# Kernel tuning notes

Measured on AMD Instinct MI355X. Metric: run time of the kernel, lower is better.

## Reference

```python
import jax, jax.numpy as jnp
import numpy as np

LATENT = 256
HEADS = 4
DIM_HEAD = 256            # dim_head = latent_channels
INNER = HEADS * DIM_HEAD  # 1024
ROT_DIM = DIM_HEAD // 2   # rotary dim per coordinate (relative_emb_dim=2)
MIN_FREQ = 1.0 / 64.0     # 1/res
ROT_SCALE = 16.0          # CrossFormer scale
FF_SCALE = 0.5            # Gaussian Fourier feature scale
PI = 3.141592653589793
OUT_CH = 3


def _gelu(x):
    return jax.nn.gelu(x, approximate=False)  # torch nn.GELU default (erf)


def _rot_freqs(coords, dim):
    # coords: [b, n] -> freqs [b, n, dim]
    inv_freq = 1.0 / (10000.0 ** (jnp.arange(0, dim, 2, dtype=jnp.float32) / dim))
    t = coords * (ROT_SCALE / MIN_FREQ)
    f = t[..., None] * inv_freq               # [b, n, dim//2]
    return jnp.concatenate([f, f], axis=-1)    # [b, n, dim]


def _rotate_half(x):
    x1, x2 = jnp.split(x, 2, axis=-1)
    return jnp.concatenate([-x2, x1], axis=-1)


def _apply_rot(t, freqs):
    return t * jnp.cos(freqs) + _rotate_half(t) * jnp.sin(freqs)


def _apply_2d_rot(t, fx, fy):
    d = t.shape[-1]
    tx, ty = t[..., : d // 2], t[..., d // 2 :]
    return jnp.concatenate([_apply_rot(tx, fx), _apply_rot(ty, fy)], axis=-1)


def _inst_norm(t, eps=1e-5):
    # galerkin normalization: non-affine norm over head dim (InstanceNorm1d, affine=False)
    mu = jnp.mean(t, axis=-1, keepdims=True)
    var = jnp.var(t, axis=-1, keepdims=True)
    return (t - mu) * jax.lax.rsqrt(var + eps)


def setup_inputs() -> dict:
    key = jax.random.key(0)
    ks = jax.random.split(key, 20)
    b, nq, nc = 8, 4096, 4096
    s = 0.02
    return {
        "z": jax.random.normal(ks[0], (b, nc, LATENT), jnp.float32),
        "query_pos": jax.random.uniform(ks[1], (b, nq, 2), jnp.float32),
        "context_pos": jax.random.uniform(ks[2], (b, nc, 2), jnp.float32),
        # GaussianFourierFeatureTransform buffer B: [2, mapping_size=latent/2]
        "B_ff": jax.random.normal(ks[3], (2, LATENT // 2), jnp.float32) * FF_SCALE,
        # coordinate_projection linears (bias=False)
        "Wc1": jax.random.normal(ks[4], (LATENT, LATENT), jnp.float32) * s,
        "Wc2": jax.random.normal(ks[5], (LATENT, LATENT), jnp.float32) * s,
        # cross attention projections
        "Wq": jax.random.normal(ks[6], (LATENT, INNER), jnp.float32) * s,
        "Wkv": jax.random.normal(ks[7], (LATENT, 2 * INNER), jnp.float32) * s,
        "Wo": jax.random.normal(ks[8], (INNER, LATENT), jnp.float32) * s,
        "bo": jnp.zeros((LATENT,), jnp.float32),
        # feed-forward (mlp_dim = latent)
        "Wf1": jax.random.normal(ks[9], (LATENT, LATENT), jnp.float32) * s,
        "bf1": jnp.zeros((LATENT,), jnp.float32),
        "Wf2": jax.random.normal(ks[10], (LATENT, LATENT), jnp.float32) * s,
        "bf2": jnp.zeros((LATENT,), jnp.float32),
        # output head
        "Wh1": jax.random.normal(ks[11], (LATENT + 2, LATENT), jnp.float32) * s,
        "Wh2": jax.random.normal(ks[12], (LATENT, LATENT // 2), jnp.float32) * s,
        "Wh3": jax.random.normal(ks[13], (LATENT // 2, OUT_CH), jnp.float32) * s,
        "bh3": jnp.zeros((OUT_CH,), jnp.float32),
    }


def reference(z, query_pos, context_pos, B_ff, Wc1, Wc2, Wq, Wkv, Wo, bo,
              Wf1, bf1, Wf2, bf2, Wh1, Wh2, Wh3, bh3):
    b, nq, _ = query_pos.shape
    nc = z.shape[1]
    # 1) Gaussian Fourier features + 2-layer projection
    ff = 2.0 * PI * (query_pos @ B_ff)                           # [b, nq, latent/2]
    x = jnp.concatenate([jnp.sin(ff), jnp.cos(ff)], axis=-1)      # [b, nq, latent]
    x = _gelu(x @ Wc1) @ Wc2
    # 2) galerkin cross attention with 2D rotary relative pos emb
    q = (x @ Wq).reshape(b, nq, HEADS, DIM_HEAD).transpose(0, 2, 1, 3)
    k, v = jnp.split(z @ Wkv, 2, axis=-1)
    k = k.reshape(b, nc, HEADS, DIM_HEAD).transpose(0, 2, 1, 3)
    v = v.reshape(b, nc, HEADS, DIM_HEAD).transpose(0, 2, 1, 3)
    fxq = _rot_freqs(query_pos[..., 0], ROT_DIM)[:, None]         # [b,1,nq,rot]
    fyq = _rot_freqs(query_pos[..., 1], ROT_DIM)[:, None]
    fxk = _rot_freqs(context_pos[..., 0], ROT_DIM)[:, None]
    fyk = _rot_freqs(context_pos[..., 1], ROT_DIM)[:, None]
    q = _apply_2d_rot(q, fxq, fyq)
    k = _apply_2d_rot(k, fxk, fyk)
    k = _inst_norm(k)
    v = _inst_norm(v)
    kv = jnp.einsum('bhnd,bhne->bhde', k, v)                      # [b,h,d,d]
    attn = jnp.einsum('bhmd,bhde->bhme', q, kv) * (1.0 / nc)      # [b,h,nq,d]
    attn = attn.transpose(0, 2, 1, 3).reshape(b, nq, INNER)
    x = (attn @ Wo + bo) + x                                      # residual
    x = (_gelu(x @ Wf1 + bf1) @ Wf2 + bf2) + x                    # FFN residual
    # 3) output head on [features, coords]
    h = jnp.concatenate([x, query_pos], axis=-1)
    h = _gelu(h @ Wh1)
    h = _gelu(h @ Wh2)
    return h @ Wh3 + bh3                                          # [b, nq, out_ch]
```

## Files before the change

### kernel.cpp

```cpp
#include <hip/hip_runtime.h>
#include <math.h>


typedef unsigned short u16;
typedef __attribute__((ext_vector_type(4))) float f32x4;
typedef __attribute__((ext_vector_type(8))) short s16x8;
typedef __attribute__((ext_vector_type(8))) unsigned short u16x8;
typedef __attribute__((ext_vector_type(4))) unsigned short u16x4;

#define LOG2_1E4_D64 0.20762050593046013f

__device__ __forceinline__ u16 f2b(float f){
  union { float f; unsigned u; } v; v.f = f;
  unsigned u = v.u;
  u += 0x7FFFu + ((u >> 16) & 1u);
  return (u16)(u >> 16);
}
__device__ __forceinline__ float b2f(u16 b){
  union { unsigned u; float f; } v; v.u = ((unsigned)b) << 16; return v.f;
}
__device__ __forceinline__ float gelu_f(float x){
  return 0.5f * x * (1.0f + erff(x * 0.7071067811865475f));
}

#if __has_builtin(__builtin_amdgcn_global_load_lds)
#define HAVE_GLL 1
typedef const __attribute__((address_space(1))) void* as1cv;
typedef __attribute__((address_space(3))) void* as3v;
__device__ __forceinline__ void gload16(const void* g, void* l){
  __builtin_amdgcn_global_load_lds((as1cv)g, (as3v)l, 16, 0, 0);
}
#else
#define HAVE_GLL 0
#endif


__global__ __launch_bounds__(256) void k_cast(const float* __restrict__ in, u16* __restrict__ out){
  long i = (long)blockIdx.x * 256 + threadIdx.x;
  float4 f = ((const float4*)in)[i];
  u16x4 o = { f2b(f.x), f2b(f.y), f2b(f.z), f2b(f.w) };
  ((u16x4*)out)[i] = o;
}

struct TCArgs {
  const float* W[9]; u16* Wt[9];
  int K[9]; int N[9]; int boff[10];
};
__global__ __launch_bounds__(256) void k_tcast_all(TCArgs a){
  int b = blockIdx.x;
  int w = 0;
  while (b >= a.boff[w+1]) w++;
  int idx = (b - a.boff[w]) * 256 + threadIdx.x;
  int K = a.K[w], N = a.N[w];
  int n = idx / K, k = idx - n * K;
  a.Wt[w][idx] = f2b(a.W[w][(long)k * N + n]);
}

__global__ __launch_bounds__(256) void k_fourier(const float* __restrict__ qp, const float* __restrict__ Bff, u16* __restrict__ X0){
  int tid = threadIdx.x;
  long r = (long)blockIdx.x * 2 + (tid >> 7);
  int j = tid & 127;
  float qx = qp[r*2], qy = qp[r*2+1];
  float ff = 6.283185307179586f * (qx * Bff[j] + qy * Bff[128 + j]);
  X0[r*256 + j]       = f2b(sinf(ff));
  X0[r*256 + 128 + j] = f2b(cosf(ff));
}

__global__ __launch_bounds__(256) void k_red(const float* __restrict__ p, u16* __restrict__ out, long stride){
  long i = (long)blockIdx.x * 256 + threadIdx.x;
  f32x4 s = ((const f32x4*)p)[i];
  s += ((const f32x4*)(p + stride))[i];
  s += ((const f32x4*)(p + 2*stride))[i];
  s += ((const f32x4*)(p + 3*stride))[i];
  u16x4 o = { f2b(s[0]), f2b(s[1]), f2b(s[2]), f2b(s[3]) };
  ((u16x4*)out)[i] = o;
}

__global__ __launch_bounds__(256) void k_final(const u16* __restrict__ H2, const float* __restrict__ Wh3,
                                               const float* __restrict__ bh3, float* __restrict__ out){
  long r = (long)blockIdx.x * 256 + threadIdx.x;
  float a0 = bh3[0], a1 = bh3[1], a2 = bh3[2];
  const u16x8* hrow = (const u16x8*)(H2 + r*128);
#pragma unroll
  for (int c8 = 0; c8 < 16; c8++){
    u16x8 hv = hrow[c8];
#pragma unroll
    for (int e = 0; e < 8; e++){
      float f = b2f(hv[e]);
      int k = c8*8 + e;
      a0 += f * Wh3[k*3];
      a1 += f * Wh3[k*3+1];
      a2 += f * Wh3[k*3+2];
    }
  }
  out[r*3] = a0; out[r*3+1] = a1; out[r*3+2] = a2;
}


template<int MODE>
__global__ __launch_bounds__(256, 2)
void gemm_fuse(const u16* __restrict__ A, const u16* __restrict__ Bw,
               u16* __restrict__ outK, u16* __restrict__ outV,
               const float* __restrict__ pos){
  __shared__ char smem[49152];
  u16* AsB[2] = { (u16*)smem,            (u16*)(smem + 8192)  };
  u16* BsB[2] = { (u16*)(smem + 16384),  (u16*)(smem + 32768) };

  int tid  = threadIdx.x;
  int lane = tid & 63;
  int wave = tid >> 6;
  int wm = (wave & 1) << 6;
  int wn = (wave >> 1) << 7;
  int whalf = wave >> 1;
  int yb = blockIdx.x;
  int h  = yb & 3;
  bool isK = (MODE == 1) || (yb < 4);
  long m0 = (long)blockIdx.y * 128;

  int r15 = lane & 15;
  int cc  = lane >> 4;
  const u16* Bh = Bw + (long)yb * 65536;

  int srow = lane >> 2;
  int scol = (lane & 3) * 8;
  int aRow[2], bRow[4];
  const u16 *gA[2], *gB[4];
#pragma unroll
  for (int t = 0; t < 2; t++){
    aRow[t] = (wave*2 + t) * 16;
    gA[t] = A + (m0 + aRow[t] + srow) * 256 + scol;
  }
#pragma unroll
  for (int t = 0; t < 4; t++){
    bRow[t] = (wave*4 + t) * 16;
    gB[t] = Bh + (bRow[t] + srow) * 256 + scol;
  }

  f32x4 acc[4][8];
#pragma unroll
  for (int i = 0; i < 4; i++)
#pragma unroll
    for (int j = 0; j < 8; j++)
      acc[i][j] = f32x4{0.f, 0.f, 0.f, 0.f};

#if HAVE_GLL
#pragma unroll
  for (int t = 0; t < 2; t++) gload16(gA[t], AsB[0] + aRow[t]*32);
#pragma unroll
  for (int t = 0; t < 4; t++) gload16(gB[t], BsB[0] + bRow[t]*32);
  __syncthreads();
  int cur = 0;
  for (int k0 = 0; k0 < 256; k0 += 32){
    int nxt = cur ^ 1;
    if (k0 < 224){
#pragma unroll
      for (int t = 0; t < 2; t++) gload16(gA[t] + k0 + 32, AsB[nxt] + aRow[t]*32);
#pragma unroll
      for (int t = 0; t < 4; t++) gload16(gB[t] + k0 + 32, BsB[nxt] + bRow[t]*32);
    }
    s16x8 af[4], bf[8];
#pragma unroll
    for (int i = 0; i < 4; i++) af[i] = *(const s16x8*)&AsB[cur][(wm + i*16 + r15)*32 + cc*8];
#pragma unroll
    for (int j = 0; j < 8; j++) bf[j] = *(const s16x8*)&BsB[cur][(wn + j*16 + r15)*32 + cc*8];
#pragma unroll
    for (int i = 0; i < 4; i++)
#pragma unroll
      for (int j = 0; j < 8; j++)
        acc[i][j] = __builtin_amdgcn_mfma_f32_16x16x32_bf16(af[i], bf[j], acc[i][j], 0, 0, 0);
    __syncthreads();
    cur = nxt;
  }
#else
  int sm = tid >> 2, sc = tid & 3;
  for (int k0 = 0; k0 < 256; k0 += 32){
    u16x8 va  = *(const u16x8*)(A + (m0 + sm)*256 + sc*8 + k0);
    u16x8 va1 = *(const u16x8*)(A + (m0 + sm + 64)*256 + sc*8 + k0);
    u16x8 vb0 = *(const u16x8*)(Bh + (sm      )*256 + sc*8 + k0);
    u16x8 vb1 = *(const u16x8*)(Bh + (sm + 64 )*256 + sc*8 + k0);
    u16x8 vb2 = *(const u16x8*)(Bh + (sm + 128)*256 + sc*8 + k0);
    u16x8 vb3 = *(const u16x8*)(Bh + (sm + 192)*256 + sc*8 + k0);
    __syncthreads();
    *(u16x8*)&AsB[0][sm*32 + sc*8] = va;
    *(u16x8*)&AsB[0][(sm+64)*32 + sc*8] = va1;
    *(u16x8*)&BsB[0][sm*32 + sc*8] = vb0;
    *(u16x8*)&BsB[0][(sm+64)*32 + sc*8] = vb1;
    *(u16x8*)&BsB[1][sm*32 + sc*8] = vb2;
    *(u16x8*)&BsB[1][(sm+64)*32 + sc*8] = vb3;
    __syncthreads();
    s16x8 af[4], bf[8];
#pragma unroll
    for (int i = 0; i < 4; i++) af[i] = *(const s16x8*)&AsB[0][(wm + i*16 + r15)*32 + cc*8];
#pragma unroll
    for (int j = 0; j < 8; j++){
      int rr = wn + j*16 + r15;
      bf[j] = (rr < 128) ? *(const s16x8*)&BsB[0][rr*32 + cc*8]
                         : *(const s16x8*)&BsB[1][(rr-128)*32 + cc*8];
    }
#pragma unroll
    for (int i = 0; i < 4; i++)
#pragma unroll
      for (int j = 0; j < 8; j++)
        acc[i][j] = __builtin_amdgcn_mfma_f32_16x16x32_bf16(af[i], bf[j], acc[i][j], 0, 0, 0);
    __syncthreads();
  }
#endif

  if (isK){
    float invf4[4];
#pragma unroll
    for (int jl = 0; jl < 4; jl++)
      invf4[jl] = 1024.0f * exp2f(-(float)(jl*16 + r15) * LOG2_1E4_D64);
#pragma unroll
    for (int i = 0; i < 4; i++){
#pragma unroll
      for (int r = 0; r < 4; r++){
        long n = m0 + wm + i*16 + cc*4 + r;
        float p = pos[n*2 + whalf];
#pragma unroll
        for (int jl = 0; jl < 4; jl++){
          float a = p * invf4[jl];
          float s = __sinf(a), c = __cosf(a);
          float t0 = acc[i][jl][r], t1 = acc[i][jl+4][r];
          acc[i][jl][r]   = t0*c - t1*s;
          acc[i][jl+4][r] = t1*c + t0*s;
        }
      }
    }
  }

  if constexpr (MODE == 1){
#pragma unroll
    for (int i = 0; i < 4; i++)
#pragma unroll
      for (int j = 0; j < 8; j++)
#pragma unroll
        for (int r = 0; r < 4; r++){
          long row = m0 + wm + i*16 + cc*4 + r;
          int col = yb*256 + wn + j*16 + r15;
          outK[row*1024 + col] = f2b(acc[i][j][r]);
        }
  } else {
    u16*   TB  = (u16*)smem;
    float* PS1 = (float*)(smem + 32768);
    float* PS2 = (float*)(smem + 33792);

#pragma unroll
    for (int i = 0; i < 4; i++){
#pragma unroll
      for (int r = 0; r < 4; r++){
        float s1 = 0.f, s2 = 0.f;
#pragma unroll
        for (int j = 0; j < 8; j++){
          float v = acc[i][j][r];
          s1 += v; s2 += v*v;
        }
#pragma unroll
        for (int m = 1; m < 16; m <<= 1){
          s1 += __shfl_xor(s1, m, 64);
          s2 += __shfl_xor(s2, m, 64);
        }
        int rowid = (wave&1)*64 + i*16 + cc*4 + r;
        if (r15 == 0){ PS1[whalf*128 + rowid] = s1; PS2[whalf*128 + rowid] = s2; }
      }
    }
    __syncthreads();
#pragma unroll
    for (int i = 0; i < 4; i++){
#pragma unroll
      for (int r = 0; r < 4; r++){
        int rowid = (wave&1)*64 + i*16 + cc*4 + r;
        float s1 = PS1[rowid] + PS1[128 + rowid];
        float s2 = PS2[rowid] + PS2[128 + rowid];
        float mu  = s1 * 0.00390625f;
        float var = s2 * 0.00390625f - mu*mu;
        float inv = 1.0f / sqrtf(var + 1e-5f);
#pragma unroll
        for (int j = 0; j < 8; j++)
          acc[i][j][r] = (acc[i][j][r] - mu) * inv;
      }
    }
    __syncthreads();

    u16* outp = isK ? outK : outV;
    int bb  = (int)(m0 >> 12);
    int nn0 = (int)(m0 & 4095);
    long matbase = ((long)(bb*4 + h) * 256) * 4096;
#pragma unroll
    for (int p = 0; p < 2; p++){
      if ((wave & 1) == p){
#pragma unroll
        for (int i = 0; i < 4; i++)
#pragma unroll
          for (int j = 0; j < 8; j++)
#pragma unroll
            for (int r = 0; r < 4; r++){
              int nl = i*16 + cc*4 + r;
              int d  = wn + j*16 + r15;
              TB[nl*256 + (d ^ ((nl>>2)<<1))] = f2b(acc[i][j][r]);
            }
      }
      __syncthreads();
      {
        int n4 = (lane & 15) * 4;
        int sw = (lane & 15) << 1;
#pragma unroll
        for (int rnd = 0; rnd < 16; rnd++){
          int d = rnd*16 + wave*4 + (lane >> 4);
          u16x4 vv;
#pragma unroll
          for (int jj = 0; jj < 4; jj++) vv[jj] = TB[(n4+jj)*256 + (d ^ sw)];
          *(u16x4*)(outp + matbase + (long)d*4096 + nn0 + p*64 + n4) = vv;
        }
      }
      __syncthreads();
    }
  }
}


enum { EP_B = 0, EP_GELU = 1, EP_BIAS_GELU = 2, EP_BIAS_RESB = 3, EP_SCALE = 4,
       EP_QP_GELU = 5, EP_F32 = 6 };

struct GArgs {
  const u16* A; const u16* B;
  u16* Cb; float* Cf;
  const float* bias; const u16* res; const float* qp; const float* wtail;
  float scale;
  int M, N, K, lda, ldb, ldc, NLO;
  long sAh, sAl, sBh, sBl, sCh, sCl;
};

template<int EP>
__global__ __launch_bounds__(256, 2)
void gemm_k(GArgs g){
  int z = blockIdx.z;
  int zh = z / g.NLO, zl = z - zh * g.NLO;
  const u16* A = g.A + (long)zh * g.sAh + (long)zl * g.sAl;
  const u16* B = g.B + (long)zh * g.sBh + (long)zl * g.sBl;
  long coff = (long)zh * g.sCh + (long)zl * g.sCl;

  __shared__ u16 As[2][128*32];
  __shared__ u16 Bs[2][128*32];

  int tid  = threadIdx.x;
  int lane = tid & 63;
  int wave = tid >> 6;
  int wm = (wave & 1) << 6;
  int wn = (wave >> 1) << 6;
  long m0 = (long)blockIdx.x * 128;
  long n0 = (long)blockIdx.y * 128;

  int r15 = lane & 15;
  int cc  = lane >> 4;

  f32x4 acc[4][4];
#pragma unroll
  for (int i = 0; i < 4; i++)
#pragma unroll
    for (int j = 0; j < 4; j++)
      acc[i][j] = f32x4{0.f, 0.f, 0.f, 0.f};

#if HAVE_GLL
  int srow = lane >> 2;
  int scol = (lane & 3) * 8;
  int aRow[2];
  const u16 *gA[2], *gB[2];
#pragma unroll
  for (int t = 0; t < 2; t++){
    aRow[t] = (wave*2 + t) * 16;
    gA[t] = A + (m0 + aRow[t] + srow) * g.lda + scol;
    gB[t] = B + (n0 + aRow[t] + srow) * g.ldb + scol;
  }
#pragma unroll
  for (int t = 0; t < 2; t++){ gload16(gA[t], As[0] + aRow[t]*32); gload16(gB[t], Bs[0] + aRow[t]*32); }
  __syncthreads();
  int cur = 0;
  for (int k0 = 0; k0 < g.K; k0 += 32){
    int nxt = cur ^ 1;
    if (k0 + 32 < g.K){
#pragma unroll
      for (int t = 0; t < 2; t++){
        gload16(gA[t] + k0 + 32, As[nxt] + aRow[t]*32);
        gload16(gB[t] + k0 + 32, Bs[nxt] + aRow[t]*32);
      }
    }
    s16x8 af[4], bf[4];
#pragma unroll
    for (int i = 0; i < 4; i++) af[i] = *(const s16x8*)&As[cur][(wm + i*16 + r15)*32 + cc*8];
#pragma unroll
    for (int i = 0; i < 4; i++) bf[i] = *(const s16x8*)&Bs[cur][(wn + i*16 + r15)*32 + cc*8];
#pragma unroll
    for (int i = 0; i < 4; i++)
#pragma unroll
      for (int j = 0; j < 4; j++)
        acc[i][j] = __builtin_amdgcn_mfma_f32_16x16x32_bf16(af[i], bf[j], acc[i][j], 0, 0, 0);
    __syncthreads();
    cur = nxt;
  }
#else
  int sm  = tid >> 2;
  int sc  = tid & 3;
  for (int k0 = 0; k0 < g.K; k0 += 32){
    u16x8 va0 = *(const u16x8*)(A + (m0 + sm )*g.lda + sc*8 + k0);
    u16x8 va1 = *(const u16x8*)(A + (m0 + sm + 64)*g.lda + sc*8 + k0);
    u16x8 vb0 = *(const u16x8*)(B + (n0 + sm )*g.ldb + sc*8 + k0);
    u16x8 vb1 = *(const u16x8*)(B + (n0 + sm + 64)*g.ldb + sc*8 + k0);
    __syncthreads();
    *(u16x8*)&As[0][sm*32 + sc*8] = va0;
    *(u16x8*)&As[0][(sm+64)*32 + sc*8] = va1;
    *(u16x8*)&Bs[0][sm*32 + sc*8] = vb0;
    *(u16x8*)&Bs[0][(sm+64)*32 + sc*8] = vb1;
    __syncthreads();
    s16x8 af[4], bf[4];
#pragma unroll
    for (int i = 0; i < 4; i++) af[i] = *(const s16x8*)&As[0][(wm + i*16 + r15)*32 + cc*8];
#pragma unroll
    for (int i = 0; i < 4; i++) bf[i] = *(const s16x8*)&Bs[0][(wn + i*16 + r15)*32 + cc*8];
#pragma unroll
    for (int i = 0; i < 4; i++)
#pragma unroll
      for (int j = 0; j < 4; j++)
        acc[i][j] = __builtin_amdgcn_mfma_f32_16x16x32_bf16(af[i], bf[j], acc[i][j], 0, 0, 0);
    __syncthreads();
  }
#endif

  int colb = (int)n0 + wn + r15;
  int rowb = (int)m0 + wm + cc * 4;
#pragma unroll
  for (int i = 0; i < 4; i++){
#pragma unroll
    for (int j = 0; j < 4; j++){
      int col = colb + j*16;
#pragma unroll
      for (int r = 0; r < 4; r++){
        int row = rowb + i*16 + r;
        float v = acc[i][j][r];
        if constexpr (EP == EP_B){
          g.Cb[coff + (long)row * g.ldc + col] = f2b(v);
        } else if constexpr (EP == EP_GELU){
          g.Cb[coff + (long)row * g.ldc + col] = f2b(gelu_f(v));
        } else if constexpr (EP == EP_BIAS_GELU){
          v = gelu_f(v + g.bias[col]);
          g.Cb[coff + (long)row * g.ldc + col] = f2b(v);
        } else if constexpr (EP == EP_BIAS_RESB){
          v += g.bias[col] + b2f(g.res[(long)row * g.ldc + col]);
          g.Cb[coff + (long)row * g.ldc + col] = f2b(v);
        } else if constexpr (EP == EP_SCALE){
          g.Cb[coff + (long)row * g.ldc + col] = f2b(v * g.scale);
        } else if constexpr (EP == EP_F32){
          g.Cf[coff + (long)row * g.ldc + col] = v;
        } else {
          v += g.qp[(long)row*2] * g.wtail[col] + g.qp[(long)row*2+1] * g.wtail[256+col];
          g.Cb[coff + (long)row * g.ldc + col] = f2b(gelu_f(v));
        }
      }
    }
  }
}


extern "C" void kernel_launch(void* const* d_in, const int* in_sizes, int n_in,
                              void* d_out, int out_size, void* d_ws, size_t ws_size,
                              hipStream_t stream){
  const float* z   = (const float*)d_in[0];
  const float* qp  = (const float*)d_in[1];
  const float* cp  = (const float*)d_in[2];
  const float* Bff = (const float*)d_in[3];
  const float* Wc1 = (const float*)d_in[4];
  const float* Wc2 = (const float*)d_in[5];
  const float* Wq  = (const float*)d_in[6];
  const float* Wkv = (const float*)d_in[7];
  const float* Wo  = (const float*)d_in[8];
  const float* bo  = (const float*)d_in[9];
  const float* Wf1 = (const float*)d_in[10];
  const float* bf1 = (const float*)d_in[11];
  const float* Wf2 = (const float*)d_in[12];
  const float* bf2 = (const float*)d_in[13];
  const float* Wh1 = (const float*)d_in[14];
  const float* Wh2 = (const float*)d_in[15];
  const float* Wh3 = (const float*)d_in[16];
  const float* bh3 = (const float*)d_in[17];
  float* out = (float*)d_out;
  (void)in_sizes; (void)n_in; (void)out_size;

  size_t mb = ws_size >> 20;
  int C;
  if      (mb >= 264) C = 1;
  else if (mb >= 168) C = 2;
  else if (mb >= 120) C = 4;
  else                C = 8;
  const int NB = 8 / C;
  const long R = (long)NB * 4096;

  char* ws = (char*)d_ws;
  const size_t MB = 1024*1024;
  u16* WqT  = (u16*)(ws + 0);
  u16* WkvT = (u16*)(ws + 512*1024);
  u16* WoT  = (u16*)(ws + 1536*1024);
  u16* Wc1T = (u16*)(ws + 2048*1024);
  u16* Wc2T = (u16*)(ws + (2048+128)*1024);
  u16* Wf1T = (u16*)(ws + (2048+256)*1024);
  u16* Wf2T = (u16*)(ws + (2048+384)*1024);
  u16* Wh1T = (u16*)(ws + (2048+512)*1024);
  u16* Wh2T = (u16*)(ws + (2048+640)*1024);
  u16* R1 = (u16*)(ws + 4*MB);
  u16* R2 = (u16*)(ws + 20*MB);
  u16* R3 = (u16*)(ws + 36*MB);
  u16* R4 = (u16*)(ws + 52*MB);
  u16* kvT = (u16*)(ws + 68*MB);
  u16* BIG1 = (u16*)(ws + 72*MB);
  u16* BIG2 = (u16*)((char*)BIG1 + (size_t)NB*8*MB);
  u16* BIG3 = (u16*)((char*)BIG2 + (size_t)NB*8*MB);

  u16* X0b = R1; u16* X2b = R1;
  u16* Tb  = R2; u16* H1b = R2;
  u16* Xb  = R3;
  u16* Zb  = R4; u16* H2b = R4;

  auto G = [&](int ep, const u16* A, const u16* B, u16* Cb, float* Cf,
               const float* bias, const u16* res, const float* qq, const float* wtail,
               float scale, int M, int N, int K, int lda, int ldb, int ldc,
               int nz, int NLO, long sAh, long sAl, long sBh, long sBl, long sCh, long sCl){
    GArgs g;
    g.A=A; g.B=B; g.Cb=Cb; g.Cf=Cf; g.bias=bias; g.res=res; g.qp=qq; g.wtail=wtail;
    g.scale=scale; g.M=M; g.N=N; g.K=K; g.lda=lda; g.ldb=ldb; g.ldc=ldc; g.NLO=NLO;
    g.sAh=sAh; g.sAl=sAl; g.sBh=sBh; g.sBl=sBl; g.sCh=sCh; g.sCl=sCl;
    dim3 gr(M/128, N/128, nz); dim3 bl(256);
    switch(ep){
      case EP_B:          gemm_k<EP_B><<<gr,bl,0,stream>>>(g); break;
      case EP_GELU:       gemm_k<EP_GELU><<<gr,bl,0,stream>>>(g); break;
      case EP_BIAS_GELU:  gemm_k<EP_BIAS_GELU><<<gr,bl,0,stream>>>(g); break;
      case EP_BIAS_RESB:  gemm_k<EP_BIAS_RESB><<<gr,bl,0,stream>>>(g); break;
      case EP_SCALE:      gemm_k<EP_SCALE><<<gr,bl,0,stream>>>(g); break;
      case EP_QP_GELU:    gemm_k<EP_QP_GELU><<<gr,bl,0,stream>>>(g); break;
      case EP_F32:        gemm_k<EP_F32><<<gr,bl,0,stream>>>(g); break;
    }
  };

  k_cast<<<dim3(8192), dim3(256), 0, stream>>>(z, Zb);
  {
    TCArgs a;
    const float* Ws[9] = { Wq, Wkv, Wo, Wc1, Wc2, Wf1, Wf2, Wh1, Wh2 };
    u16* Wts[9] = { WqT, WkvT, WoT, Wc1T, Wc2T, Wf1T, Wf2T, Wh1T, Wh2T };
    int Ks[9] = { 256, 256, 1024, 256, 256, 256, 256, 256, 256 };
    int Ns[9] = { 1024, 2048, 256, 256, 256, 256, 256, 256, 128 };
    int off = 0;
    for (int i = 0; i < 9; i++){
      a.W[i] = Ws[i]; a.Wt[i] = Wts[i]; a.K[i] = Ks[i]; a.N[i] = Ns[i];
      a.boff[i] = off; off += Ks[i]*Ns[i]/256;
    }
    a.boff[9] = off;
    k_tcast_all<<<dim3(off), dim3(256), 0, stream>>>(a);
  }

  k_fourier<<<dim3(16384), dim3(256), 0, stream>>>(qp, Bff, X0b);
  G(EP_GELU, X0b, Wc1T, Tb, 0, 0,0,0,0, 1.f, 32768,256,256, 256,256,256, 1,1, 0,0,0,0,0,0);
  G(EP_B,    Tb,  Wc2T, Xb, 0, 0,0,0,0, 1.f, 32768,256,256, 256,256,256, 1,1, 0,0,0,0,0,0);

  for (int c = 0; c < C; c++){
    long row0 = (long)c * R;
    const u16* Zc = Zb + row0 * 256;
    gemm_fuse<0><<<dim3(8, (int)(R/128)), dim3(256), 0, stream>>>(Zc, WkvT, BIG2, BIG3, cp + row0*2);
    G(EP_F32, BIG3, BIG2, 0, (float*)BIG1, 0,0,0,0, 1.f,
      256,256,1024, 4096,4096,256, 4*NB*4, NB*4,
      1024,1048576, 1024,1048576, (long)NB*4*65536,65536);
    k_red<<<dim3(NB*256), dim3(256), 0, stream>>>((float*)BIG1, kvT + (long)c*NB*4*65536, (long)NB*4*65536);
    gemm_fuse<1><<<dim3(4, (int)(R/128)), dim3(256), 0, stream>>>(Xb + row0*256, WqT, BIG1, 0, qp + row0*2);
    G(EP_SCALE, BIG1, kvT + (long)c*NB*4*65536, BIG2, 0, 0,0,0,0, 1.0f/4096.0f,
      4096,256,256, 1024,256,1024, NB*4,4, 4194304,256, 262144,65536, 4194304,256);
    G(EP_BIAS_RESB, BIG2, WoT, X2b + row0*256, 0, bo, Xb + row0*256, 0,0, 1.f,
      (int)R,256,1024, 1024,1024,256, 1,1, 0,0,0,0,0,0);
  }

  G(EP_BIAS_GELU, X2b, Wf1T, Tb, 0, bf1, 0,0,0, 1.f, 32768,256,256, 256,256,256, 1,1, 0,0,0,0,0,0);
  G(EP_BIAS_RESB, Tb, Wf2T, Xb, 0, bf2, X2b, 0,0, 1.f, 32768,256,256, 256,256,256, 1,1, 0,0,0,0,0,0);
  G(EP_QP_GELU, Xb, Wh1T, H1b, 0, 0,0, qp, Wh1 + 65536, 1.f, 32768,256,256, 256,256,256, 1,1, 0,0,0,0,0,0);
  G(EP_GELU, H1b, Wh2T, H2b, 0, 0,0,0,0, 1.f, 32768,128,256, 256,256,128, 1,1, 0,0,0,0,0,0);
  k_final<<<dim3(128), dim3(256), 0, stream>>>(H2b, Wh3, bh3, out);
}
```

Before: 540.4 us.

## Deepen GEMM prefetch with vmcnt waits, swizzle LDS, merge prep kernels

The GEMM main loops now stage two k-tiles ahead and wait on explicit vmcnt counters with raw barriers, instead of a full __syncthreads after every tile. This lets global-to-LDS loads overlap compute for longer. LDS columns are XOR-swizzled on both the load and fragment-read side to cut bank conflicts. The z cast, weight transpose-cast and Fourier feature kernels are merged into one prep launch to save launch overhead. The hand-written waitcnt/sched_barrier sequencing is fragile, so an extra sync was added before the epilogue reuses shared memory.

Measured after the change: 526.6 us. -2.6%, faster.

```diff
diff --git a/kernel.cpp b/kernel.cpp
--- a/kernel.cpp
+++ b/kernel.cpp
@@ -9,6 +9,11 @@
 typedef __attribute__((ext_vector_type(4))) unsigned short u16x4;
 
 #define LOG2_1E4_D64 0.20762050593046013f
+
+#define VMCNT(n) do{ asm volatile("s_waitcnt vmcnt(" #n ")" ::: "memory"); \
+                     __builtin_amdgcn_sched_barrier(0); }while(0)
+#define BARRIER() do{ __builtin_amdgcn_s_barrier(); \
+                      __builtin_amdgcn_sched_barrier(0); }while(0)
 
 __device__ __forceinline__ u16 f2b(float f){
   union { float f; unsigned u; } v; v.f = f;
@@ -35,35 +40,37 @@
 #endif
 
 
-__global__ __launch_bounds__(256) void k_cast(const float* __restrict__ in, u16* __restrict__ out){
-  long i = (long)blockIdx.x * 256 + threadIdx.x;
-  float4 f = ((const float4*)in)[i];
-  u16x4 o = { f2b(f.x), f2b(f.y), f2b(f.z), f2b(f.w) };
-  ((u16x4*)out)[i] = o;
-}
-
-struct TCArgs {
+struct PrepArgs {
+  const float* z; u16* Zb;
+  const float* qp; const float* Bff; u16* X0;
   const float* W[9]; u16* Wt[9];
   int K[9]; int N[9]; int boff[10];
+  int castB, tcB;
 };
-__global__ __launch_bounds__(256) void k_tcast_all(TCArgs a){
-  int b = blockIdx.x;
-  int w = 0;
-  while (b >= a.boff[w+1]) w++;
-  int idx = (b - a.boff[w]) * 256 + threadIdx.x;
-  int K = a.K[w], N = a.N[w];
-  int n = idx / K, k = idx - n * K;
-  a.Wt[w][idx] = f2b(a.W[w][(long)k * N + n]);
-}
-
-__global__ __launch_bounds__(256) void k_fourier(const float* __restrict__ qp, const float* __restrict__ Bff, u16* __restrict__ X0){
-  int tid = threadIdx.x;
-  long r = (long)blockIdx.x * 2 + (tid >> 7);
-  int j = tid & 127;
-  float qx = qp[r*2], qy = qp[r*2+1];
-  float ff = 6.283185307179586f * (qx * Bff[j] + qy * Bff[128 + j]);
-  X0[r*256 + j]       = f2b(sinf(ff));
-  X0[r*256 + 128 + j] = f2b(cosf(ff));
+__global__ __launch_bounds__(256) void k_prep(PrepArgs a){
+  int b = blockIdx.x, tid = threadIdx.x;
+  if (b < a.castB){
+    long i = (long)b * 256 + tid;
+    float4 f = ((const float4*)a.z)[i];
+    u16x4 o = { f2b(f.x), f2b(f.y), f2b(f.z), f2b(f.w) };
+    ((u16x4*)a.Zb)[i] = o;
+  } else if (b < a.castB + a.tcB){
+    int bb = b - a.castB;
+    int w = 0;
+    while (bb >= a.boff[w+1]) w++;
+    int idx = (bb - a.boff[w]) * 256 + tid;
+    int K = a.K[w], N = a.N[w];
+    int n = idx / K, k = idx - n * K;
+    a.Wt[w][idx] = f2b(a.W[w][(long)k * N + n]);
+  } else {
+    int bb = b - a.castB - a.tcB;
+    long r = (long)bb * 2 + (tid >> 7);
+    int j = tid & 127;
+    float qx = a.qp[r*2], qy = a.qp[r*2+1];
+    float ff = 6.283185307179586f * (qx * a.Bff[j] + qy * a.Bff[128 + j]);
+    a.X0[r*256 + j]       = f2b(sinf(ff));
+    a.X0[r*256 + 128 + j] = f2b(cosf(ff));
+  }
 }
 
 __global__ __launch_bounds__(256) void k_red(const float* __restrict__ p, u16* __restrict__ out, long stride){
@@ -103,8 +110,8 @@
                u16* __restrict__ outK, u16* __restrict__ outV,
                const float* __restrict__ pos){
   __shared__ char smem[49152];
-  u16* AsB[2] = { (u16*)smem,            (u16*)(smem + 8192)  };
-  u16* BsB[2] = { (u16*)(smem + 16384),  (u16*)(smem + 32768) };
+  u16* AsB = (u16*)smem;
+  u16* BsB = (u16*)(smem + 16384);
 
   int tid  = threadIdx.x;
   int lane = tid & 63;
@@ -119,58 +126,69 @@
 
   int r15 = lane & 15;
   int cc  = lane >> 4;
+  int fsw = (cc ^ ((r15 >> 1) & 3)) * 8;
   const u16* Bh = Bw + (long)yb * 65536;
 
-  int srow = lane >> 2;
-  int scol = (lane & 3) * 8;
+  f32x4 acc[4][8];
+#pragma unroll
+  for (int i = 0; i < 4; i++)
+#pragma unroll
+    for (int j = 0; j < 8; j++)
+      acc[i][j] = f32x4{0.f, 0.f, 0.f, 0.f};
+
+#if HAVE_GLL
+  int srow  = lane >> 2;
+  int scolS = ((lane & 3) ^ ((lane >> 3) & 3)) * 8;
   int aRow[2], bRow[4];
   const u16 *gA[2], *gB[4];
 #pragma unroll
   for (int t = 0; t < 2; t++){
     aRow[t] = (wave*2 + t) * 16;
-    gA[t] = A + (m0 + aRow[t] + srow) * 256 + scol;
+    gA[t] = A + (m0 + aRow[t] + srow) * 256 + scolS;
   }
 #pragma unroll
   for (int t = 0; t < 4; t++){
     bRow[t] = (wave*4 + t) * 16;
-    gB[t] = Bh + (bRow[t] + srow) * 256 + scol;
-  }
-
-  f32x4 acc[4][8];
-#pragma unroll
-  for (int i = 0; i < 4; i++)
-#pragma unroll
-    for (int j = 0; j < 8; j++)
-      acc[i][j] = f32x4{0.f, 0.f, 0.f, 0.f};
-
-#if HAVE_GLL
-#pragma unroll
-  for (int t = 0; t < 2; t++) gload16(gA[t], AsB[0] + aRow[t]*32);
-#pragma unroll
-  for (int t = 0; t < 4; t++) gload16(gB[t], BsB[0] + bRow[t]*32);
-  __syncthreads();
-  int cur = 0;
-  for (int k0 = 0; k0 < 256; k0 += 32){
-    int nxt = cur ^ 1;
-    if (k0 < 224){
-#pragma unroll
-      for (int t = 0; t < 2; t++) gload16(gA[t] + k0 + 32, AsB[nxt] + aRow[t]*32);
-#pragma unroll
-      for (int t = 0; t < 4; t++) gload16(gB[t] + k0 + 32, BsB[nxt] + bRow[t]*32);
-    }
+    gB[t] = Bh + (bRow[t] + srow) * 256 + scolS;
+  }
+  auto stage = [&](int buf, int kk){
+    u16* ab = AsB + buf*4096;
+    u16* bb = BsB + buf*8192;
+#pragma unroll
+    for (int t = 0; t < 2; t++) gload16(gA[t] + kk*32, ab + aRow[t]*32);
+#pragma unroll
+    for (int t = 0; t < 4; t++) gload16(gB[t] + kk*32, bb + bRow[t]*32);
+  };
+  auto compute = [&](int buf){
+    const u16* ab = AsB + buf*4096;
+    const u16* bb = BsB + buf*8192;
     s16x8 af[4], bf[8];
 #pragma unroll
-    for (int i = 0; i < 4; i++) af[i] = *(const s16x8*)&AsB[cur][(wm + i*16 + r15)*32 + cc*8];
-#pragma unroll
-    for (int j = 0; j < 8; j++) bf[j] = *(const s16x8*)&BsB[cur][(wn + j*16 + r15)*32 + cc*8];
+    for (int i = 0; i < 4; i++) af[i] = *(const s16x8*)&ab[(wm + i*16 + r15)*32 + fsw];
+#pragma unroll
+    for (int j = 0; j < 8; j++) bf[j] = *(const s16x8*)&bb[(wn + j*16 + r15)*32 + fsw];
 #pragma unroll
     for (int i = 0; i < 4; i++)
 #pragma unroll
       for (int j = 0; j < 8; j++)
         acc[i][j] = __builtin_amdgcn_mfma_f32_16x16x32_bf16(af[i], bf[j], acc[i][j], 0, 0, 0);
-    __syncthreads();
-    cur = nxt;
-  }
+  };
+
+  stage(0, 0);
+  stage(1, 1);
+  int cur = 0;
+  for (int t = 0; t < 7; t++){
+    VMCNT(6);
+    BARRIER();
+    compute(cur);
+    __builtin_amdgcn_sched_barrier(0);
+    BARRIER();
+    if (t + 2 < 8) stage(cur, t + 2);
+    cur ^= 1;
+  }
+  VMCNT(0);
+  BARRIER();
+  compute(cur);
 #else
   int sm = tid >> 2, sc = tid & 3;
   for (int k0 = 0; k0 < 256; k0 += 32){
@@ -181,22 +199,18 @@
     u16x8 vb2 = *(const u16x8*)(Bh + (sm + 128)*256 + sc*8 + k0);
     u16x8 vb3 = *(const u16x8*)(Bh + (sm + 192)*256 + sc*8 + k0);
     __syncthreads();
-    *(u16x8*)&AsB[0][sm*32 + sc*8] = va;
-    *(u16x8*)&AsB[0][(sm+64)*32 + sc*8] = va1;
-    *(u16x8*)&BsB[0][sm*32 + sc*8] = vb0;
-    *(u16x8*)&BsB[0][(sm+64)*32 + sc*8] = vb1;
-    *(u16x8*)&BsB[1][sm*32 + sc*8] = vb2;
-    *(u16x8*)&BsB[1][(sm+64)*32 + sc*8] = vb3;
+    *(u16x8*)&AsB[sm*32 + sc*8] = va;
+    *(u16x8*)&AsB[(sm+64)*32 + sc*8] = va1;
+    *(u16x8*)&BsB[sm*32 + sc*8] = vb0;
+    *(u16x8*)&BsB[(sm+64)*32 + sc*8] = vb1;
+    *(u16x8*)&BsB[(sm+128)*32 + sc*8] = vb2;
+    *(u16x8*)&BsB[(sm+192)*32 + sc*8] = vb3;
     __syncthreads();
     s16x8 af[4], bf[8];
 #pragma unroll
-    for (int i = 0; i < 4; i++) af[i] = *(const s16x8*)&AsB[0][(wm + i*16 + r15)*32 + cc*8];
-#pragma unroll
-    for (int j = 0; j < 8; j++){
-      int rr = wn + j*16 + r15;
-      bf[j] = (rr < 128) ? *(const s16x8*)&BsB[0][rr*32 + cc*8]
-                         : *(const s16x8*)&BsB[1][(rr-128)*32 + cc*8];
-    }
+    for (int i = 0; i < 4; i++) af[i] = *(const s16x8*)&AsB[(wm + i*16 + r15)*32 + cc*8];
+#pragma unroll
+    for (int j = 0; j < 8; j++) bf[j] = *(const s16x8*)&BsB[(wn + j*16 + r15)*32 + cc*8];
 #pragma unroll
     for (int i = 0; i < 4; i++)
 #pragma unroll
@@ -244,6 +258,8 @@
     u16*   TB  = (u16*)smem;
     float* PS1 = (float*)(smem + 32768);
     float* PS2 = (float*)(smem + 33792);
+
+    __syncthreads();
 
 #pragma unroll
     for (int i = 0; i < 4; i++){
@@ -353,6 +369,7 @@
 
   int r15 = lane & 15;
   int cc  = lane >> 4;
+  int fsw = (cc ^ ((r15 >> 1) & 3)) * 8;
 
   f32x4 acc[4][4];
 #pragma unroll
@@ -362,42 +379,52 @@
       acc[i][j] = f32x4{0.f, 0.f, 0.f, 0.f};
 
 #if HAVE_GLL
-  int srow = lane >> 2;
-  int scol = (lane & 3) * 8;
+  int srow  = lane >> 2;
+  int scolS = ((lane & 3) ^ ((lane >> 3) & 3)) * 8;
   int aRow[2];
   const u16 *gA[2], *gB[2];
 #pragma unroll
   for (int t = 0; t < 2; t++){
     aRow[t] = (wave*2 + t) * 16;
-    gA[t] = A + (m0 + aRow[t] + srow) * g.lda + scol;
-    gB[t] = B + (n0 + aRow[t] + srow) * g.ldb + scol;
-  }
-#pragma unroll
-  for (int t = 0; t < 2; t++){ gload16(gA[t], As[0] + aRow[t]*32); gload16(gB[t], Bs[0] + aRow[t]*32); }
-  __syncthreads();
-  int cur = 0;
-  for (int k0 = 0; k0 < g.K; k0 += 32){
-    int nxt = cur ^ 1;
-    if (k0 + 32 < g.K){
-#pragma unroll
-      for (int t = 0; t < 2; t++){
-        gload16(gA[t] + k0 + 32, As[nxt] + aRow[t]*32);
-        gload16(gB[t] + k0 + 32, Bs[nxt] + aRow[t]*32);
-      }
-    }
+    gA[t] = A + (m0 + aRow[t] + srow) * g.lda + scolS;
+    gB[t] = B + (n0 + aRow[t] + srow) * g.ldb + scolS;
+  }
+  auto stage = [&](int buf, int kk){
+#pragma unroll
+    for (int t = 0; t < 2; t++){
+      gload16(gA[t] + kk*32, &As[buf][aRow[t]*32]);
+      gload16(gB[t] + kk*32, &Bs[buf][aRow[t]*32]);
+    }
+  };
+  auto compute = [&](int buf){
     s16x8 af[4], bf[4];
 #pragma unroll
-    for (int i = 0; i < 4; i++) af[i] = *(const s16x8*)&As[cur][(wm + i*16 + r15)*32 + cc*8];
-#pragma unroll
-    for (int i = 0; i < 4; i++) bf[i] = *(const s16x8*)&Bs[cur][(wn + i*16 + r15)*32 + cc*8];
+    for (int i = 0; i < 4; i++) af[i] = *(const s16x8*)&As[buf][(wm + i*16 + r15)*32 + fsw];
+#pragma unroll
+    for (int i = 0; i < 4; i++) bf[i] = *(const s16x8*)&Bs[buf][(wn + i*16 + r15)*32 + fsw];
 #pragma unroll
     for (int i = 0; i < 4; i++)
 #pragma unroll
       for (int j = 0; j < 4; j++)
         acc[i][j] = __builtin_amdgcn_mfma_f32_16x16x32_bf16(af[i], bf[j], acc[i][j], 0, 0, 0);
-    __syncthreads();
-    cur = nxt;
-  }
+  };
+
+  int nt = g.K >> 5;
+  stage(0, 0);
+  stage(1, 1);
+  int cur = 0;
+  for (int t = 0; t < nt - 1; t++){
+    VMCNT(4);
+    BARRIER();
+    compute(cur);
+    __builtin_amdgcn_sched_barrier(0);
+    BARRIER();
+    if (t + 2 < nt) stage(cur, t + 2);
+    cur ^= 1;
+  }
+  VMCNT(0);
+  BARRIER();
+  compute(cur);
 #else
   int sm  = tid >> 2;
   int sc  = tid & 3;
@@ -539,9 +566,9 @@
     }
   };
 
-  k_cast<<<dim3(8192), dim3(256), 0, stream>>>(z, Zb);
   {
-    TCArgs a;
+    PrepArgs a;
+    a.z = z; a.Zb = Zb; a.qp = qp; a.Bff = Bff; a.X0 = X0b;
     const float* Ws[9] = { Wq, Wkv, Wo, Wc1, Wc2, Wf1, Wf2, Wh1, Wh2 };
     u16* Wts[9] = { WqT, WkvT, WoT, Wc1T, Wc2T, Wf1T, Wf2T, Wh1T, Wh2T };
     int Ks[9] = { 256, 256, 1024, 256, 256, 256, 256, 256, 256 };
@@ -552,10 +579,10 @@
       a.boff[i] = off; off += Ks[i]*Ns[i]/256;
     }
     a.boff[9] = off;
-    k_tcast_all<<<dim3(off), dim3(256), 0, stream>>>(a);
-  }
-
-  k_fourier<<<dim3(16384), dim3(256), 0, stream>>>(qp, Bff, X0b);
+    a.castB = 8192; a.tcB = off;
+    k_prep<<<dim3(8192 + off + 16384), dim3(256), 0, stream>>>(a);
+  }
+
   G(EP_GELU, X0b, Wc1T, Tb, 0, 0,0,0,0, 1.f, 32768,256,256, 256,256,256, 1,1, 0,0,0,0,0,0);
   G(EP_B,    Tb,  Wc2T, Xb, 0, 0,0,0,0, 1.f, 32768,256,256, 256,256,256, 1,1, 0,0,0,0,0,0);
 
```
